# Kernel optimization log

Measured on AMD Instinct MI355X. Metric: run time of the kernel, lower is better.

The kernel has to match this reference:

```python
import jax, jax.numpy as jnp
import numpy as np

EPS = 1e-5


def _selective_scan(u, delta, A, Bm, Cm, D, delta_bias):
    # u, delta: (B, KD, L); A: (KD, N); Bm, Cm: (B, K, N, L); D, delta_bias: (KD,)
    Bb, KD, L = u.shape
    K = Bm.shape[1]
    Din = KD // K
    N = A.shape[1]
    delta = jax.nn.softplus(delta + delta_bias[None, :, None])            # (B,KD,L)
    dA = jnp.exp(delta[..., None] * A[None, :, None, :])                  # (B,KD,L,N)
    Bl = jnp.broadcast_to(Bm[:, :, None], (Bb, K, Din, N, L)).reshape(Bb, KD, N, L)
    Bl = jnp.moveaxis(Bl, -1, 2)                                          # (B,KD,L,N)
    dBu = (delta * u)[..., None] * Bl                                     # (B,KD,L,N)

    def comb(c1, c2):
        a1, b1 = c1
        a2, b2 = c2
        return a2 * a1, a2 * b1 + b2

    _, h = jax.lax.associative_scan(comb, (dA, dBu), axis=2)              # h: (B,KD,L,N)
    Cl = jnp.broadcast_to(Cm[:, :, None], (Bb, K, Din, N, L)).reshape(Bb, KD, N, L)
    Cl = jnp.moveaxis(Cl, -1, 2)
    y = jnp.sum(h * Cl, axis=-1) + D[None, :, None] * u                   # (B,KD,L)
    return y


def setup_inputs() -> dict:
    key = jax.random.key(0)
    ks = jax.random.split(key, 12)
    B, H, W, Dd = 1, 16, 16, 16
    C = 48            # d_model
    Din = 48          # d_inner (expand=1)
    N = 16            # d_state
    R = 3             # dt_rank = ceil(48/16)
    K = 8             # scan directions
    x = jax.random.normal(ks[0], (B, H, W, Dd, C), jnp.float32)
    in_proj_w = jax.random.normal(ks[1], (2 * Din, C), jnp.float32) * (C ** -0.5)
    conv_w = jax.random.normal(ks[2], (Din, 1, 3, 3, 3), jnp.float32) * 0.1
    conv_b = jax.random.normal(ks[3], (Din,), jnp.float32) * 0.01
    x_proj_weight = jax.random.normal(ks[4], (K, R + 2 * N, Din), jnp.float32) * (Din ** -0.5)
    dt_projs_weight = jax.random.uniform(ks[5], (K, Din, R), jnp.float32, -(R ** -0.5), R ** -0.5)
    # faithful dt bias init: inverse softplus of dt ~ logU(1e-3, 1e-1)
    u = jax.random.uniform(ks[6], (K, Din), jnp.float32)
    dt = jnp.exp(u * (np.log(0.1) - np.log(0.001)) + np.log(0.001))
    dt = jnp.clip(dt, 1e-4, None)
    dt_projs_bias = dt + jnp.log(-jnp.expm1(-dt))
    A_logs = jnp.log(jnp.broadcast_to(jnp.arange(1, N + 1, dtype=jnp.float32), (K * Din, N))).copy()
    Ds = jnp.ones((K * Din,), jnp.float32)
    norm_w = jnp.ones((Din,), jnp.float32)
    norm_b = jnp.zeros((Din,), jnp.float32)
    out_proj_w = jax.random.normal(ks[7], (C, Din), jnp.float32) * (Din ** -0.5)
    return {"x": x, "in_proj_w": in_proj_w, "conv_w": conv_w, "conv_b": conv_b,
            "x_proj_weight": x_proj_weight, "dt_projs_weight": dt_projs_weight,
            "dt_projs_bias": dt_projs_bias, "A_logs": A_logs, "Ds": Ds,
            "norm_w": norm_w, "norm_b": norm_b, "out_proj_w": out_proj_w}


def reference(x, in_proj_w, conv_w, conv_b, x_proj_weight, dt_projs_weight,
              dt_projs_bias, A_logs, Ds, norm_w, norm_b, out_proj_w):
    Bb, H, W, Dd, C = x.shape
    Din = in_proj_w.shape[0] // 2
    K = x_proj_weight.shape[0]
    R = dt_projs_weight.shape[2]
    N = A_logs.shape[1]
    L = H * W * Dd
    # in_proj and gate split
    xz = jnp.einsum('bhwdc,ec->bhwde', x, in_proj_w)
    xm, z = jnp.split(xz, 2, axis=-1)
    # depthwise 3D conv + SiLU (channels-first)
    xc = jnp.transpose(xm, (0, 4, 1, 2, 3))                               # (B,Din,H,W,D)
    xc = jax.lax.conv_general_dilated(xc, conv_w, (1, 1, 1), 'SAME',
                                      dimension_numbers=('NCDHW', 'OIDHW', 'NCDHW'),
                                      feature_group_count=Din)
    xc = jax.nn.silu(xc + conv_b[None, :, None, None, None])
    # 8 scan orderings: 4 axis permutations + their reversals
    x0 = xc.reshape(Bb, Din, L)
    x1 = jnp.transpose(xc, (0, 1, 3, 2, 4)).reshape(Bb, Din, L)
    x2 = jnp.transpose(xc, (0, 1, 4, 3, 2)).reshape(Bb, Din, L)
    x3 = jnp.transpose(xc, (0, 1, 2, 4, 3)).reshape(Bb, Din, L)
    x4s = jnp.stack([x0, x1, x2, x3], axis=1)                             # (B,4,Din,L)
    xs = jnp.concatenate([x4s, jnp.flip(x4s, axis=-1)], axis=1)           # (B,8,Din,L)
    # per-direction projections
    x_dbl = jnp.einsum('bkdl,kcd->bkcl', xs, x_proj_weight)
    dts, Bs, Cs = jnp.split(x_dbl, [R, R + N], axis=2)                    # (B,K,R,L),(B,K,N,L),(B,K,N,L)
    dts = jnp.einsum('bkrl,kdr->bkdl', dts, dt_projs_weight)              # (B,K,Din,L)
    u = xs.reshape(Bb, K * Din, L)
    delta = dts.reshape(Bb, K * Din, L)
    A = -jnp.exp(A_logs)                                                  # (K*Din, N)
    y = _selective_scan(u, delta, A, Bs, Cs, Ds, dt_projs_bias.reshape(-1))
    y = y.reshape(Bb, K, Din, L)
    # undo reversals and permutations, sum all directions
    yk = y[:, :4] + jnp.flip(y[:, 4:], axis=-1)                           # (B,4,Din,L)
    y0 = yk[:, 0].reshape(Bb, Din, H, W, Dd)
    y1 = jnp.transpose(yk[:, 1].reshape(Bb, Din, W, H, Dd), (0, 1, 3, 2, 4))
    y2 = jnp.transpose(yk[:, 2].reshape(Bb, Din, Dd, W, H), (0, 1, 4, 3, 2))
    y3 = jnp.transpose(yk[:, 3].reshape(Bb, Din, H, Dd, W), (0, 1, 2, 4, 3))
    ysum = y0 + y1 + y2 + y3                                              # (B,Din,H,W,D)
    # LayerNorm over channels, gate, out_proj
    yl = jnp.transpose(ysum, (0, 2, 3, 4, 1))                             # (B,H,W,D,Din)
    mu = jnp.mean(yl, axis=-1, keepdims=True)
    var = jnp.mean((yl - mu) ** 2, axis=-1, keepdims=True)
    yn = (yl - mu) * jax.lax.rsqrt(var + EPS) * norm_w + norm_b
    out = yn * jax.nn.silu(z)
    return jnp.einsum('bhwde,ce->bhwdc', out, out_proj_w)
```

## Files before the change

### kernel.cpp

```cpp
#include <hip/hip_runtime.h>
#include <hip/hip_bf16.h>
#include <math.h>

#define HH 16
#define WW 16
#define DD 16
#define LL 4096
#define CC 48
#define DIN 48
#define NN 16
#define RR 3
#define KK 8
#define KD 384
#define NCH 64
#define CHL 64

__device__ __forceinline__ float dpp_add(float x, const int ctrl_tag) {
    int xi = __float_as_int(x);
    int yi;
    switch (ctrl_tag) {
        case 0: yi = __builtin_amdgcn_update_dpp(0, xi, 0xB1, 0xF, 0xF, true); break;
        case 1: yi = __builtin_amdgcn_update_dpp(0, xi, 0x4E, 0xF, 0xF, true); break;
        case 2: yi = __builtin_amdgcn_update_dpp(0, xi, 0x124, 0xF, 0xF, true); break;
        default: yi = __builtin_amdgcn_update_dpp(0, xi, 0x128, 0xF, 0xF, true); break;
    }
    return x + __int_as_float(yi);
}
__device__ __forceinline__ float row16_sum(float p) {
    p = dpp_add(p, 0);
    p = dpp_add(p, 1);
    p = dpp_add(p, 2);
    p = dpp_add(p, 3);
    return p;
}

__global__ __launch_bounds__(256) void k_inproj(const float* __restrict__ x,
                                                const float* __restrict__ W,
                                                float* __restrict__ xm,
                                                float* __restrict__ z) {
    int tid = blockIdx.x * 256 + threadIdx.x;
    if (tid >= LL * 96) return;
    int e = tid % 96, l = tid / 96;
    const float4* xr = (const float4*)(x + l * CC);
    const float4* wr = (const float4*)(W + e * CC);
    float acc = 0.f;
#pragma unroll
    for (int c4 = 0; c4 < CC / 4; ++c4) {
        float4 a = xr[c4], b = wr[c4];
        acc += a.x * b.x + a.y * b.y + a.z * b.z + a.w * b.w;
    }
    if (e < DIN) xm[e * LL + l] = acc;
    else         z[l * DIN + (e - DIN)] = acc;
}

__global__ __launch_bounds__(256) void k_conv(const float* __restrict__ xm,
                                              const float* __restrict__ cw,
                                              const float* __restrict__ cb,
                                              float* __restrict__ xc) {
    int tid = blockIdx.x * 256 + threadIdx.x;
    if (tid >= DIN * LL) return;
    int s = tid & (LL - 1), d = tid >> 12;
    int dd = s & 15, w = (s >> 4) & 15, h = s >> 8;
    const float* wp = cw + d * 27;
    const float* xp = xm + d * LL;
    float acc = 0.f;
#pragma unroll
    for (int i = -1; i <= 1; ++i) {
        int hh = h + i; if (hh < 0 || hh > 15) continue;
#pragma unroll
        for (int j = -1; j <= 1; ++j) {
            int ww2 = w + j; if (ww2 < 0 || ww2 > 15) continue;
#pragma unroll
            for (int q = -1; q <= 1; ++q) {
                int dd2 = dd + q; if (dd2 < 0 || dd2 > 15) continue;
                acc += wp[(i + 1) * 9 + (j + 1) * 3 + (q + 1)]
                     * xp[hh * 256 + ww2 * 16 + dd2];
            }
        }
    }
    acc += cb[d];
    xc[tid] = acc / (1.f + __expf(-acc));
}

__global__ __launch_bounds__(768) void k_xscan1(const float* __restrict__ xc,
                                                const float* __restrict__ xpw,
                                                const float* __restrict__ dtw,
                                                const float* __restrict__ dtb,
                                                const float* __restrict__ A_logs,
                                                float* __restrict__ BC,
                                                float* __restrict__ ud_g,
                                                float* __restrict__ pa_g,
                                                float* __restrict__ hf_g) {
    int k = blockIdx.x >> 6;
    int c = blockIdx.x & (NCH - 1);
    int l0 = c * CHL;
    int tid = threadIdx.x;
    __shared__ float xt[48 * 68];
    __shared__ float xd[35 * 65];
    __shared__ float2 ud[48 * 68];
    int kperm = k & 3, krev = k & 4;
#pragma unroll
    for (int r = 0; r < 4; ++r) {
        int item = r * 768 + tid;
        int d = item >> 6, i = item & 63;
        int lg = l0 + i;
        int ll = krev ? (LL - 1 - lg) : lg;
        int a = ll >> 8, b2 = (ll >> 4) & 15, c2 = ll & 15;
        int src;
        switch (kperm) {
            case 0: src = ll;                       break;
            case 1: src = b2 * 256 + a * 16 + c2;   break;
            case 2: src = c2 * 256 + b2 * 16 + a;   break;
            default: src = a * 256 + c2 * 16 + b2;  break;
        }
        xt[d * 68 + i] = xc[d * LL + src];
    }
    __syncthreads();
    if (tid < 560) {
        int cc = tid % 35, l4 = tid / 35;
        const float* wr = xpw + (k * 35 + cc) * DIN;
        float4 acc = {0.f, 0.f, 0.f, 0.f};
#pragma unroll
        for (int d2 = 0; d2 < 48; ++d2) {
            float4 v = ((const float4*)(xt + d2 * 68))[l4];
            float w = wr[d2];
            acc.x += v.x * w; acc.y += v.y * w; acc.z += v.z * w; acc.w += v.w * w;
        }
        float* o = xd + cc * 65 + l4 * 4;
        o[0] = acc.x; o[1] = acc.y; o[2] = acc.z; o[3] = acc.w;
    }
    __syncthreads();
    if (tid < 512) {
        int l = tid >> 3, q = tid & 7;
        float4 v;
#pragma unroll
        for (int j = 0; j < 4; ++j) (&v.x)[j] = xd[(3 + q * 4 + j) * 65 + l];
        ((float4*)(BC + ((size_t)(k * LL + l0 + l)) * 32))[q] = v;
    }
#pragma unroll
    for (int r = 0; r < 4; ++r) {
        int item = r * 768 + tid;
        int d2 = item >> 6, l = item & 63;
        int gd = k * DIN + d2;
        float v = xd[l] * dtw[gd * 3] + xd[65 + l] * dtw[gd * 3 + 1]
                + xd[130 + l] * dtw[gd * 3 + 2] + dtb[gd];
        float sp = (v > 20.f) ? v : log1pf(__expf(v));
        float u = xt[d2 * 68 + l];
        float2 p = make_float2(u, sp);
        ud[d2 * 68 + l] = p;
        ((float2*)ud_g)[(size_t)gd * LL + l0 + l] = p;
    }
    __syncthreads();
    int d = tid >> 4, n = tid & 15;
    int gid = k * DIN + d;
    float A = -__expf(A_logs[gid * NN + n]);
    float h = 0.f, pa = 1.f;
#pragma unroll 8
    for (int i = 0; i < CHL; ++i) {
        float2 uv = ud[d * 68 + i];
        float Bv = xd[(3 + n) * 65 + i];
        float dA = __expf(uv.y * A);
        h = h * dA + uv.y * uv.x * Bv;
        pa *= dA;
    }
    size_t si = (size_t)gid * (NCH * 16) + c * 16 + n;
    pa_g[si] = pa;
    hf_g[si] = h;
}

__global__ __launch_bounds__(256) void k_scan2(const float* __restrict__ pa_g,
                                               const float* __restrict__ hf_g,
                                               float* __restrict__ h0_g) {
    int t = blockIdx.x * 256 + threadIdx.x;
    if (t >= KD * NN) return;
    int n = t & 15;
    int gid = t >> 4;
    size_t base = (size_t)gid * (NCH * 16) + n;
    float h = 0.f;
#pragma unroll 4
    for (int c = 0; c < NCH; ++c) {
        size_t idx = base + (size_t)c * 16;
        h0_g[idx] = h;
        h = h * pa_g[idx] + hf_g[idx];
    }
}

__global__ __launch_bounds__(768) void k_scan3(const float* __restrict__ ud_g,
                                               const float* __restrict__ BC,
                                               const float* __restrict__ A_logs,
                                               const float* __restrict__ Ds,
                                               const float* __restrict__ h0_g,
                                               float* __restrict__ y2) {
    int k = blockIdx.x >> 6;
    int c = blockIdx.x & (NCH - 1);
    int l0 = c * CHL;
    int tid = threadIdx.x;
    int d = tid >> 4, n = tid & 15;
    int gid = k * DIN + d;
    __shared__ float y_t[48 * 68];
    float A = -__expf(A_logs[gid * NN + n]);
    float Dv = Ds[gid];
    float h = h0_g[(size_t)gid * (NCH * 16) + c * 16 + n];
    const float2* up = ((const float2*)ud_g) + (size_t)gid * LL + l0;
    const float* bp = BC + ((size_t)(k * LL + l0)) * 32 + n;
    const float* cp = bp + 16;
#pragma unroll 8
    for (int i = 0; i < CHL; ++i) {
        float2 uv = up[i];
        float Bv = bp[(size_t)i * 32];
        float Cv = cp[(size_t)i * 32];
        float dA = __expf(uv.y * A);
        h = h * dA + uv.y * uv.x * Bv;
        float p = row16_sum(h * Cv);
        if (n == 0) y_t[d * 68 + i] = p + Dv * uv.x;
    }
    __syncthreads();
    {
        int g = tid >> 6, l = tid & 63;
        int lg = l0 + l;
        int ll = (k & 4) ? (LL - 1 - lg) : lg;
        int a = ll >> 8, b2 = (ll >> 4) & 15, c2 = ll & 15;
        int s;
        switch (k & 3) {
            case 0: s = ll;                        break;
            case 1: s = b2 * 256 + a * 16 + c2;    break;
            case 2: s = c2 * 256 + b2 * 16 + a;    break;
            default: s = a * 256 + c2 * 16 + b2;   break;
        }
        float4 v;
#pragma unroll
        for (int j = 0; j < 4; ++j) (&v.x)[j] = y_t[(g * 4 + j) * 68 + l];
        ((float4*)(y2 + (size_t)s * KD + k * DIN))[g] = v;
    }
}

__global__ __launch_bounds__(256) void k_final2(const float* __restrict__ y2,
                                                const float* __restrict__ z,
                                                const float* __restrict__ nw,
                                                const float* __restrict__ nb,
                                                const float* __restrict__ opw,
                                                float* __restrict__ out) {
    int wv = threadIdx.x >> 6, lane = threadIdx.x & 63;
    int s = blockIdx.x * 4 + wv;
    __shared__ float g[4][DIN];
    float val = 0.f;
    if (lane < DIN) {
        const float* yp = y2 + (size_t)s * KD + lane;
#pragma unroll
        for (int k = 0; k < KK; ++k) val += yp[k * DIN];
    }
    float m = val;
#pragma unroll
    for (int o = 32; o >= 1; o >>= 1) m += __shfl_xor(m, o, 64);
    m *= (1.f / 48.f);
    float dv = (lane < DIN) ? (val - m) : 0.f;
    float v2 = dv * dv;
#pragma unroll
    for (int o = 32; o >= 1; o >>= 1) v2 += __shfl_xor(v2, o, 64);
    v2 *= (1.f / 48.f);
    float inv = rsqrtf(v2 + 1e-5f);
    if (lane < DIN) {
        float yn = dv * inv * nw[lane] + nb[lane];
        float zz = z[s * DIN + lane];
        g[wv][lane] = yn * (zz / (1.f + __expf(-zz)));
    }
    __syncthreads();
    if (lane < DIN) {
        const float* wr = opw + lane * DIN;
        float acc = 0.f;
#pragma unroll
        for (int e = 0; e < DIN; ++e) acc += g[wv][e] * wr[e];
        out[s * CC + lane] = acc;
    }
}

extern "C" void kernel_launch(void* const* d_in, const int* in_sizes, int n_in,
                              void* d_out, int out_size, void* d_ws, size_t ws_size,
                              hipStream_t stream) {
    const float* x      = (const float*)d_in[0];
    const float* ipw    = (const float*)d_in[1];
    const float* cw     = (const float*)d_in[2];
    const float* cb     = (const float*)d_in[3];
    const float* xpw    = (const float*)d_in[4];
    const float* dtw    = (const float*)d_in[5];
    const float* dtb    = (const float*)d_in[6];
    const float* A_logs = (const float*)d_in[7];
    const float* Ds     = (const float*)d_in[8];
    const float* nw     = (const float*)d_in[9];
    const float* nb     = (const float*)d_in[10];
    const float* opw    = (const float*)d_in[11];
    float* out = (float*)d_out;

    float* ws   = (float*)d_ws;
    float* xm   = ws;
    float* z    = xm + DIN * LL;
    float* xc   = z + LL * DIN;
    float* ud_g = xc + DIN * LL;
    float* BC   = ud_g + (size_t)2 * KD * LL;
    float* y2   = BC + (size_t)KK * LL * 32;
    float* pa_g = y2 + (size_t)LL * KD;
    float* hf_g = pa_g + (size_t)KD * NCH * 16;
    float* h0_g = hf_g + (size_t)KD * NCH * 16;

    k_inproj<<<(LL * 96 + 255) / 256, 256, 0, stream>>>(x, ipw, xm, z);
    k_conv<<<(DIN * LL + 255) / 256, 256, 0, stream>>>(xm, cw, cb, xc);
    k_xscan1<<<KK * NCH, 768, 0, stream>>>(xc, xpw, dtw, dtb, A_logs,
                                           BC, ud_g, pa_g, hf_g);
    k_scan2<<<(KD * NN + 255) / 256, 256, 0, stream>>>(pa_g, hf_g, h0_g);
    k_scan3<<<KK * NCH, 768, 0, stream>>>(ud_g, BC, A_logs, Ds, h0_g, y2);
    k_final2<<<LL / 4, 256, 0, stream>>>(y2, z, nw, nb, opw, out);
}
```

Baseline: 156.3 us.

## Fuse scan pipeline and final norm into one cooperative kernel with grid syncs

Replaces the four-kernel scan chain (chunk scan, carry scan, output scan, layernorm/out-proj) with a single cooperative kernel of 256 blocks. Each block handles a forward and a reversed direction for one chunk, recomputes x_proj and dt in shared memory instead of spilling ud/BC to global, and gets its carry-in by serially folding the prefix chunk summaries after a grid sync. Launch overhead and the large global intermediates go away, but the extra front-end recompute, the serial per-block prefix loop, heavy shared memory use limiting occupancy, and grid-wide barriers are added. If the cooperative launch fails, it falls back to unfused kernels that also recompute the front end.

Measured after the change: 229.4 us. +46.8%, slower.

```diff
diff --git a/kernel.cpp b/kernel.cpp
--- a/kernel.cpp
+++ b/kernel.cpp
@@ -1,6 +1,8 @@
 #include <hip/hip_runtime.h>
-#include <hip/hip_bf16.h>
+#include <hip/hip_cooperative_groups.h>
 #include <math.h>
+
+namespace cg = cooperative_groups;
 
 #define HH 16
 #define WW 16
@@ -34,6 +36,16 @@
     return p;
 }
 
+__device__ __forceinline__ int perm_src(int ll, int kperm) {
+    int a = ll >> 8, b2 = (ll >> 4) & 15, c2 = ll & 15;
+    switch (kperm) {
+        case 0:  return ll;
+        case 1:  return b2 * 256 + a * 16 + c2;
+        case 2:  return c2 * 256 + b2 * 16 + a;
+        default: return a * 256 + c2 * 16 + b2;
+    }
+}
+
 __global__ __launch_bounds__(256) void k_inproj(const float* __restrict__ x,
                                                 const float* __restrict__ W,
                                                 float* __restrict__ xm,
@@ -82,22 +94,12 @@
     xc[tid] = acc / (1.f + __expf(-acc));
 }
 
-__global__ __launch_bounds__(768) void k_xscan1(const float* __restrict__ xc,
-                                                const float* __restrict__ xpw,
-                                                const float* __restrict__ dtw,
-                                                const float* __restrict__ dtb,
-                                                const float* __restrict__ A_logs,
-                                                float* __restrict__ BC,
-                                                float* __restrict__ ud_g,
-                                                float* __restrict__ pa_g,
-                                                float* __restrict__ hf_g) {
-    int k = blockIdx.x >> 6;
-    int c = blockIdx.x & (NCH - 1);
-    int l0 = c * CHL;
-    int tid = threadIdx.x;
-    __shared__ float xt[48 * 68];
-    __shared__ float xd[35 * 65];
-    __shared__ float2 ud[48 * 68];
+__device__ __forceinline__ void frontend(const float* __restrict__ xc,
+                                         const float* __restrict__ xpw,
+                                         const float* __restrict__ dtw,
+                                         const float* __restrict__ dtb,
+                                         int k, int l0, int tid,
+                                         float* xt, float* xd, float2* ud) {
     int kperm = k & 3, krev = k & 4;
 #pragma unroll
     for (int r = 0; r < 4; ++r) {
@@ -105,15 +107,7 @@
         int d = item >> 6, i = item & 63;
         int lg = l0 + i;
         int ll = krev ? (LL - 1 - lg) : lg;
-        int a = ll >> 8, b2 = (ll >> 4) & 15, c2 = ll & 15;
-        int src;
-        switch (kperm) {
-            case 0: src = ll;                       break;
-            case 1: src = b2 * 256 + a * 16 + c2;   break;
-            case 2: src = c2 * 256 + b2 * 16 + a;   break;
-            default: src = a * 256 + c2 * 16 + b2;  break;
-        }
-        xt[d * 68 + i] = xc[d * LL + src];
+        xt[d * 68 + i] = xc[d * LL + perm_src(ll, kperm)];
     }
     __syncthreads();
     if (tid < 560) {
@@ -130,13 +124,6 @@
         o[0] = acc.x; o[1] = acc.y; o[2] = acc.z; o[3] = acc.w;
     }
     __syncthreads();
-    if (tid < 512) {
-        int l = tid >> 3, q = tid & 7;
-        float4 v;
-#pragma unroll
-        for (int j = 0; j < 4; ++j) (&v.x)[j] = xd[(3 + q * 4 + j) * 65 + l];
-        ((float4*)(BC + ((size_t)(k * LL + l0 + l)) * 32))[q] = v;
-    }
 #pragma unroll
     for (int r = 0; r < 4; ++r) {
         int item = r * 768 + tid;
@@ -145,12 +132,155 @@
         float v = xd[l] * dtw[gd * 3] + xd[65 + l] * dtw[gd * 3 + 1]
                 + xd[130 + l] * dtw[gd * 3 + 2] + dtb[gd];
         float sp = (v > 20.f) ? v : log1pf(__expf(v));
-        float u = xt[d2 * 68 + l];
-        float2 p = make_float2(u, sp);
-        ud[d2 * 68 + l] = p;
-        ((float2*)ud_g)[(size_t)gd * LL + l0 + l] = p;
-    }
-    __syncthreads();
+        ud[d2 * 68 + l] = make_float2(xt[d2 * 68 + l], sp);
+    }
+    __syncthreads();
+}
+
+__device__ __forceinline__ void phase3_store(const float2* ud, const float* xd,
+                                             float A, float Dv, float hseed,
+                                             int d, int n, int tid, int k,
+                                             int l0, float* y_t,
+                                             float* __restrict__ y2) {
+    float h = hseed;
+#pragma unroll 8
+    for (int i = 0; i < CHL; ++i) {
+        float2 uv = ud[d * 68 + i];
+        float Bv = xd[(3 + n) * 65 + i];
+        float Cv = xd[(19 + n) * 65 + i];
+        float dA = __expf(uv.y * A);
+        h = h * dA + uv.y * uv.x * Bv;
+        float p = row16_sum(h * Cv);
+        if (n == 0) y_t[d * 68 + i] = p + Dv * uv.x;
+    }
+    __syncthreads();
+    int g2 = tid >> 6, l = tid & 63;
+    int lg = l0 + l;
+    int ll = (k & 4) ? (LL - 1 - lg) : lg;
+    int sp = perm_src(ll, k & 3);
+    float4 v;
+#pragma unroll
+    for (int j = 0; j < 4; ++j) (&v.x)[j] = y_t[(g2 * 4 + j) * 68 + l];
+    ((float4*)(y2 + (size_t)sp * KD + k * DIN))[g2] = v;
+    __syncthreads();
+}
+
+__global__ __launch_bounds__(768, 3) void k_scan_fused(
+        const float* __restrict__ xc,  const float* __restrict__ xpw,
+        const float* __restrict__ dtw, const float* __restrict__ dtb,
+        const float* __restrict__ A_logs, const float* __restrict__ Ds,
+        const float* __restrict__ z,   const float* __restrict__ nw,
+        const float* __restrict__ nb,  const float* __restrict__ opw,
+        float* __restrict__ pa_g, float* __restrict__ hf_g,
+        float* __restrict__ y2,   float* __restrict__ out) {
+    cg::grid_group grid = cg::this_grid();
+    int k0 = blockIdx.x >> 6;
+    int c  = blockIdx.x & (NCH - 1);
+    int l0 = c * CHL;
+    int tid = threadIdx.x;
+    int d = tid >> 4, n = tid & 15;
+    __shared__ float  xt[48 * 68];
+    __shared__ float  xd0[35 * 65], xd1[35 * 65];
+    __shared__ float2 ud0[48 * 68], ud1[48 * 68];
+
+    frontend(xc, xpw, dtw, dtb, k0,     l0, tid, xt, xd0, ud0);
+    frontend(xc, xpw, dtw, dtb, k0 + 4, l0, tid, xt, xd1, ud1);
+
+    int gid0 = k0 * DIN + d, gid1 = (k0 + 4) * DIN + d;
+    float A0 = -__expf(A_logs[gid0 * NN + n]);
+    float A1 = -__expf(A_logs[gid1 * NN + n]);
+    {
+        float h0 = 0.f, pa0 = 1.f, h1 = 0.f, pa1 = 1.f;
+#pragma unroll 4
+        for (int i = 0; i < CHL; ++i) {
+            float2 u0 = ud0[d * 68 + i];
+            float2 u1 = ud1[d * 68 + i];
+            float B0 = xd0[(3 + n) * 65 + i];
+            float B1 = xd1[(3 + n) * 65 + i];
+            float dA0 = __expf(u0.y * A0);
+            float dA1 = __expf(u1.y * A1);
+            h0 = h0 * dA0 + u0.y * u0.x * B0; pa0 *= dA0;
+            h1 = h1 * dA1 + u1.y * u1.x * B1; pa1 *= dA1;
+        }
+        size_t si0 = (size_t)gid0 * (NCH * 16) + c * 16 + n;
+        size_t si1 = (size_t)gid1 * (NCH * 16) + c * 16 + n;
+        pa_g[si0] = pa0; hf_g[si0] = h0;
+        pa_g[si1] = pa1; hf_g[si1] = h1;
+    }
+
+    grid.sync();
+
+    float s0 = 0.f, s1 = 0.f;
+    {
+        size_t b0 = (size_t)gid0 * (NCH * 16) + n;
+        size_t b1 = (size_t)gid1 * (NCH * 16) + n;
+        for (int cc = 0; cc < c; ++cc) {
+            size_t i0 = b0 + (size_t)cc * 16;
+            size_t i1 = b1 + (size_t)cc * 16;
+            s0 = s0 * pa_g[i0] + hf_g[i0];
+            s1 = s1 * pa_g[i1] + hf_g[i1];
+        }
+    }
+    phase3_store(ud0, xd0, A0, Ds[gid0], s0, d, n, tid, k0,     l0, xt, y2);
+    phase3_store(ud1, xd1, A1, Ds[gid1], s1, d, n, tid, k0 + 4, l0, xt, y2);
+
+    grid.sync();
+
+    int wv = tid >> 6, lane = tid & 63;
+    float* gbuf = xd0;
+#pragma unroll
+    for (int rep = 0; rep < 2; ++rep) {
+        int s = blockIdx.x * 16 + rep * 8 + wv;
+        bool act = (wv < 8);
+        float val = 0.f;
+        if (act && lane < DIN) {
+            const float* yp = y2 + (size_t)s * KD + lane;
+#pragma unroll
+            for (int kk = 0; kk < KK; ++kk) val += yp[kk * DIN];
+        }
+        float m = val;
+#pragma unroll
+        for (int o = 32; o >= 1; o >>= 1) m += __shfl_xor(m, o, 64);
+        m *= (1.f / 48.f);
+        float dvv = (act && lane < DIN) ? (val - m) : 0.f;
+        float v2 = dvv * dvv;
+#pragma unroll
+        for (int o = 32; o >= 1; o >>= 1) v2 += __shfl_xor(v2, o, 64);
+        v2 *= (1.f / 48.f);
+        float inv = rsqrtf(v2 + 1e-5f);
+        if (act && lane < DIN) {
+            float yn = dvv * inv * nw[lane] + nb[lane];
+            float zz = z[(size_t)s * DIN + lane];
+            gbuf[wv * DIN + lane] = yn * (zz / (1.f + __expf(-zz)));
+        }
+        __syncthreads();
+        if (act && lane < DIN) {
+            const float* wr = opw + lane * DIN;
+            float acc = 0.f;
+#pragma unroll
+            for (int e = 0; e < DIN; ++e) acc += gbuf[wv * DIN + e] * wr[e];
+            out[(size_t)s * CC + lane] = acc;
+        }
+        __syncthreads();
+    }
+}
+
+
+__global__ __launch_bounds__(768) void k_scanA(const float* __restrict__ xc,
+                                               const float* __restrict__ xpw,
+                                               const float* __restrict__ dtw,
+                                               const float* __restrict__ dtb,
+                                               const float* __restrict__ A_logs,
+                                               float* __restrict__ pa_g,
+                                               float* __restrict__ hf_g) {
+    int k = blockIdx.x >> 6;
+    int c = blockIdx.x & (NCH - 1);
+    int l0 = c * CHL;
+    int tid = threadIdx.x;
+    __shared__ float  xt[48 * 68];
+    __shared__ float  xd[35 * 65];
+    __shared__ float2 ud[48 * 68];
+    frontend(xc, xpw, dtw, dtb, k, l0, tid, xt, xd, ud);
     int d = tid >> 4, n = tid & 15;
     int gid = k * DIN + d;
     float A = -__expf(A_logs[gid * NN + n]);
@@ -185,8 +315,10 @@
     }
 }
 
-__global__ __launch_bounds__(768) void k_scan3(const float* __restrict__ ud_g,
-                                               const float* __restrict__ BC,
+__global__ __launch_bounds__(768) void k_scanB(const float* __restrict__ xc,
+                                               const float* __restrict__ xpw,
+                                               const float* __restrict__ dtw,
+                                               const float* __restrict__ dtb,
                                                const float* __restrict__ A_logs,
                                                const float* __restrict__ Ds,
                                                const float* __restrict__ h0_g,
@@ -195,43 +327,15 @@
     int c = blockIdx.x & (NCH - 1);
     int l0 = c * CHL;
     int tid = threadIdx.x;
+    __shared__ float  xt[48 * 68];
+    __shared__ float  xd[35 * 65];
+    __shared__ float2 ud[48 * 68];
+    frontend(xc, xpw, dtw, dtb, k, l0, tid, xt, xd, ud);
     int d = tid >> 4, n = tid & 15;
     int gid = k * DIN + d;
-    __shared__ float y_t[48 * 68];
     float A = -__expf(A_logs[gid * NN + n]);
-    float Dv = Ds[gid];
-    float h = h0_g[(size_t)gid * (NCH * 16) + c * 16 + n];
-    const float2* up = ((const float2*)ud_g) + (size_t)gid * LL + l0;
-    const float* bp = BC + ((size_t)(k * LL + l0)) * 32 + n;
-    const float* cp = bp + 16;
-#pragma unroll 8
-    for (int i = 0; i < CHL; ++i) {
-        float2 uv = up[i];
-        float Bv = bp[(size_t)i * 32];
-        float Cv = cp[(size_t)i * 32];
-        float dA = __expf(uv.y * A);
-        h = h * dA + uv.y * uv.x * Bv;
-        float p = row16_sum(h * Cv);
-        if (n == 0) y_t[d * 68 + i] = p + Dv * uv.x;
-    }
-    __syncthreads();
-    {
-        int g = tid >> 6, l = tid & 63;
-        int lg = l0 + l;
-        int ll = (k & 4) ? (LL - 1 - lg) : lg;
-        int a = ll >> 8, b2 = (ll >> 4) & 15, c2 = ll & 15;
-        int s;
-        switch (k & 3) {
-            case 0: s = ll;                        break;
-            case 1: s = b2 * 256 + a * 16 + c2;    break;
-            case 2: s = c2 * 256 + b2 * 16 + a;    break;
-            default: s = a * 256 + c2 * 16 + b2;   break;
-        }
-        float4 v;
-#pragma unroll
-        for (int j = 0; j < 4; ++j) (&v.x)[j] = y_t[(g * 4 + j) * 68 + l];
-        ((float4*)(y2 + (size_t)s * KD + k * DIN))[g] = v;
-    }
+    float hs = h0_g[(size_t)gid * (NCH * 16) + c * 16 + n];
+    phase3_store(ud, xd, A, Ds[gid], hs, d, n, tid, k, l0, xt, y2);
 }
 
 __global__ __launch_bounds__(256) void k_final2(const float* __restrict__ y2,
@@ -295,18 +399,27 @@
     float* xm   = ws;
     float* z    = xm + DIN * LL;
     float* xc   = z + LL * DIN;
-    float* ud_g = xc + DIN * LL;
-    float* BC   = ud_g + (size_t)2 * KD * LL;
-    float* y2   = BC + (size_t)KK * LL * 32;
+    float* y2   = xc + DIN * LL;
     float* pa_g = y2 + (size_t)LL * KD;
     float* hf_g = pa_g + (size_t)KD * NCH * 16;
     float* h0_g = hf_g + (size_t)KD * NCH * 16;
 
     k_inproj<<<(LL * 96 + 255) / 256, 256, 0, stream>>>(x, ipw, xm, z);
     k_conv<<<(DIN * LL + 255) / 256, 256, 0, stream>>>(xm, cw, cb, xc);
-    k_xscan1<<<KK * NCH, 768, 0, stream>>>(xc, xpw, dtw, dtb, A_logs,
-                                           BC, ud_g, pa_g, hf_g);
-    k_scan2<<<(KD * NN + 255) / 256, 256, 0, stream>>>(pa_g, hf_g, h0_g);
-    k_scan3<<<KK * NCH, 768, 0, stream>>>(ud_g, BC, A_logs, Ds, h0_g, y2);
-    k_final2<<<LL / 4, 256, 0, stream>>>(y2, z, nw, nb, opw, out);
-}
+
+    void* args[] = {(void*)&xc, (void*)&xpw, (void*)&dtw, (void*)&dtb,
+                    (void*)&A_logs, (void*)&Ds, (void*)&z, (void*)&nw,
+                    (void*)&nb, (void*)&opw, (void*)&pa_g, (void*)&hf_g,
+                    (void*)&y2, (void*)&out};
+    hipError_t ce = hipLaunchCooperativeKernel((void*)k_scan_fused,
+                                               dim3(256), dim3(768),
+                                               args, 0, stream);
+    if (ce != hipSuccess) {
+        k_scanA<<<KK * NCH, 768, 0, stream>>>(xc, xpw, dtw, dtb, A_logs,
+                                              pa_g, hf_g);
+        k_scan2<<<(KD * NN + 255) / 256, 256, 0, stream>>>(pa_g, hf_g, h0_g);
+        k_scanB<<<KK * NCH, 768, 0, stream>>>(xc, xpw, dtw, dtb, A_logs, Ds,
+                                              h0_g, y2);
+        k_final2<<<LL / 4, 256, 0, stream>>>(y2, z, nw, nb, opw, out);
+    }
+}
```

## Fold inter-chunk carry scan into scan3, removing the separate scan2 kernel

Applied to the files above, without the earlier changes.

Drops the standalone chunk-carry propagation kernel. Each scan3 thread now recomputes its initial state by serially combining the (decay, final state) pairs of all preceding chunks, read as interleaved float2. This removes one kernel launch and the global round trip through the h0 buffer. In exchange there is redundant serial work, up to 63 dependent loads per thread for late chunks, which adds latency to those blocks.

Result: slower. 164.5 us (+5.3%).

```diff
diff --git a/kernel.cpp b/kernel.cpp
--- a/kernel.cpp
+++ b/kernel.cpp
@@ -89,8 +89,7 @@
                                                 const float* __restrict__ A_logs,
                                                 float* __restrict__ BC,
                                                 float* __restrict__ ud_g,
-                                                float* __restrict__ pa_g,
-                                                float* __restrict__ hf_g) {
+                                                float* __restrict__ phf_g) {
     int k = blockIdx.x >> 6;
     int c = blockIdx.x & (NCH - 1);
     int l0 = c * CHL;
@@ -164,32 +163,14 @@
         pa *= dA;
     }
     size_t si = (size_t)gid * (NCH * 16) + c * 16 + n;
-    pa_g[si] = pa;
-    hf_g[si] = h;
-}
-
-__global__ __launch_bounds__(256) void k_scan2(const float* __restrict__ pa_g,
-                                               const float* __restrict__ hf_g,
-                                               float* __restrict__ h0_g) {
-    int t = blockIdx.x * 256 + threadIdx.x;
-    if (t >= KD * NN) return;
-    int n = t & 15;
-    int gid = t >> 4;
-    size_t base = (size_t)gid * (NCH * 16) + n;
-    float h = 0.f;
-#pragma unroll 4
-    for (int c = 0; c < NCH; ++c) {
-        size_t idx = base + (size_t)c * 16;
-        h0_g[idx] = h;
-        h = h * pa_g[idx] + hf_g[idx];
-    }
+    ((float2*)phf_g)[si] = make_float2(pa, h);
 }
 
 __global__ __launch_bounds__(768) void k_scan3(const float* __restrict__ ud_g,
                                                const float* __restrict__ BC,
                                                const float* __restrict__ A_logs,
                                                const float* __restrict__ Ds,
-                                               const float* __restrict__ h0_g,
+                                               const float* __restrict__ phf_g,
                                                float* __restrict__ y2) {
     int k = blockIdx.x >> 6;
     int c = blockIdx.x & (NCH - 1);
@@ -200,7 +181,14 @@
     __shared__ float y_t[48 * 68];
     float A = -__expf(A_logs[gid * NN + n]);
     float Dv = Ds[gid];
-    float h = h0_g[(size_t)gid * (NCH * 16) + c * 16 + n];
+    float h = 0.f;
+    {
+        const float2* pp = ((const float2*)phf_g) + (size_t)gid * (NCH * 16) + n;
+        for (int cc = 0; cc < c; ++cc) {
+            float2 v = pp[cc * 16];
+            h = h * v.x + v.y;
+        }
+    }
     const float2* up = ((const float2*)ud_g) + (size_t)gid * LL + l0;
     const float* bp = BC + ((size_t)(k * LL + l0)) * 32 + n;
     const float* cp = bp + 16;
@@ -291,22 +279,19 @@
     const float* opw    = (const float*)d_in[11];
     float* out = (float*)d_out;
 
-    float* ws   = (float*)d_ws;
-    float* xm   = ws;
-    float* z    = xm + DIN * LL;
-    float* xc   = z + LL * DIN;
-    float* ud_g = xc + DIN * LL;
-    float* BC   = ud_g + (size_t)2 * KD * LL;
-    float* y2   = BC + (size_t)KK * LL * 32;
-    float* pa_g = y2 + (size_t)LL * KD;
-    float* hf_g = pa_g + (size_t)KD * NCH * 16;
-    float* h0_g = hf_g + (size_t)KD * NCH * 16;
+    float* ws    = (float*)d_ws;
+    float* xm    = ws;
+    float* z     = xm + DIN * LL;
+    float* xc    = z + LL * DIN;
+    float* ud_g  = xc + DIN * LL;
+    float* BC    = ud_g + (size_t)2 * KD * LL;
+    float* y2    = BC + (size_t)KK * LL * 32;
+    float* phf_g = y2 + (size_t)LL * KD;
 
     k_inproj<<<(LL * 96 + 255) / 256, 256, 0, stream>>>(x, ipw, xm, z);
     k_conv<<<(DIN * LL + 255) / 256, 256, 0, stream>>>(xm, cw, cb, xc);
     k_xscan1<<<KK * NCH, 768, 0, stream>>>(xc, xpw, dtw, dtb, A_logs,
-                                           BC, ud_g, pa_g, hf_g);
-    k_scan2<<<(KD * NN + 255) / 256, 256, 0, stream>>>(pa_g, hf_g, h0_g);
-    k_scan3<<<KK * NCH, 768, 0, stream>>>(ud_g, BC, A_logs, Ds, h0_g, y2);
+                                           BC, ud_g, phf_g);
+    k_scan3<<<KK * NCH, 768, 0, stream>>>(ud_g, BC, A_logs, Ds, phf_g, y2);
     k_final2<<<LL / 4, 256, 0, stream>>>(y2, z, nw, nb, opw, out);
 }
```
